# Kernel tuning notes

Hardware: AMD Instinct MI355X
Metric: run time of the kernel (lower is better)

The kernel has to match this reference:

```python
import jax, jax.numpy as jnp
import numpy as np

EPS = 1e-8
TEMP = 0.05

def setup_inputs() -> dict:
    key = jax.random.key(0)
    ks = jax.random.split(key, 7)
    B, S, IN, OUT, R, K = 4, 4096, 4096, 4096, 8, 4
    x = jax.random.normal(ks[0], (B, S, IN), dtype=jnp.float32)
    V_shared = jax.random.normal(ks[1], (R, IN), dtype=jnp.float32) * 0.01
    U_shared = jax.random.normal(ks[2], (OUT, R), dtype=jnp.float32) * 0.01
    core_pool = jax.random.normal(ks[3], (K, R, R), dtype=jnp.float32)
    core_keys = jax.random.normal(ks[4], (K, IN), dtype=jnp.float32)
    gate_w = jax.random.normal(ks[5], (1, 2 * R), dtype=jnp.float32) * 0.1
    gate_b = jnp.ones((1,), dtype=jnp.float32)
    return {"x": x, "V_shared": V_shared, "U_shared": U_shared,
            "core_pool": core_pool, "core_keys": core_keys,
            "gate_w": gate_w, "gate_b": gate_b}

def reference(x, V_shared, U_shared, core_pool, core_keys, gate_w, gate_b):
    # --- Hebbian cosine router (eval mode: keys are fixed buffers) ---
    centroid = 0.7 * x[:, -1, :] + 0.3 * jnp.mean(x, axis=1)          # [B, in]
    cn = centroid / jnp.maximum(jnp.linalg.norm(centroid, axis=-1, keepdims=True), EPS)
    kn = core_keys / jnp.maximum(jnp.linalg.norm(core_keys, axis=-1, keepdims=True), EPS)
    sim = cn @ kn.T                                                     # [B, K]
    route_weights = jax.nn.softmax(sim / TEMP, axis=-1)                 # [B, K]
    # --- Soft core mixture: per-batch rank x rank matrix ---
    Lam_active = jnp.einsum('bk,kij->bij', route_weights, core_pool)    # [B, r, r]
    # --- Low-rank chain: x @ V^T @ Lam^T @ U^T ---
    x_V = jnp.einsum('bsi,ri->bsr', x, V_shared)                        # [B, S, r]
    x_V_Lam = jnp.einsum('bsr,bjr->bsj', x_V, Lam_active)               # bmm with Lam^T
    adapt_out = jnp.einsum('bsj,oj->bso', x_V_Lam, U_shared)            # [B, S, out]
    # --- GainLoRA sigmoid gate (scalar), gate input detached ---
    gate_in = jax.lax.stop_gradient(
        jnp.concatenate([U_shared.mean(axis=0), V_shared.mean(axis=1)], axis=0))  # [2r]
    gate = jax.nn.sigmoid(gate_w @ gate_in + gate_b)                    # [1]
    return gate[0] * adapt_out
```

## Files before the change

### kernel.cpp

```cpp
#include <hip/hip_runtime.h>
#include <math.h>

#define B_   4
#define S_   4096
#define IN_  4096
#define OUT_ 4096
#define RNK  8
#define K_   4

#define NBLK_A 512

__global__ __launch_bounds__(256) void zK(float* __restrict__ p) {
    p[blockIdx.x * 256 + threadIdx.x] = 0.f;
}

__global__ __launch_bounds__(512) void kA(const float* __restrict__ x,
                                          const float* __restrict__ V,
                                          float* __restrict__ colsum,
                                          float* __restrict__ xv)
{
    __shared__ float shcs[IN_];
    const int tid = threadIdx.x;
    for (int c = tid; c < IN_; c += 512) shcs[c] = 0.f;
    __syncthreads();

    const int blk  = blockIdx.x;
    const int b    = blk >> 7;
    const int sblk = blk & 127;
    const int w = tid >> 6, l = tid & 63, g = l >> 4, j = l & 15;
    const int s = sblk * 32 + w * 4 + g;
    const float* xr = x + ((size_t)(b * S_ + s)) * IN_;

    float p[8] = {0.f,0.f,0.f,0.f,0.f,0.f,0.f,0.f};
    #pragma unroll 4
    for (int chunk = 0; chunk < 64; ++chunk) {
        const int col = chunk * 64 + j * 4;
        const float4 x4 = *(const float4*)(xr + col);
        #pragma unroll
        for (int r = 0; r < 8; ++r) {
            const float4 v4 = *(const float4*)(V + r * IN_ + col);
            p[r] += x4.x * v4.x + x4.y * v4.y + x4.z * v4.z + x4.w * v4.w;
        }
        float c0 = x4.x, c1 = x4.y, c2 = x4.z, c3 = x4.w;
        c0 += __shfl_xor(c0, 16); c1 += __shfl_xor(c1, 16);
        c2 += __shfl_xor(c2, 16); c3 += __shfl_xor(c3, 16);
        c0 += __shfl_xor(c0, 32); c1 += __shfl_xor(c1, 32);
        c2 += __shfl_xor(c2, 32); c3 += __shfl_xor(c3, 32);
        if (l < 16) {
            atomicAdd(&shcs[col + 0], c0);
            atomicAdd(&shcs[col + 1], c1);
            atomicAdd(&shcs[col + 2], c2);
            atomicAdd(&shcs[col + 3], c3);
        }
    }

    #pragma unroll
    for (int m = 1; m <= 8; m <<= 1) {
        #pragma unroll
        for (int r = 0; r < 8; ++r) p[r] += __shfl_xor(p[r], m);
    }
    float* xvp = xv + ((size_t)(b * S_ + s)) * RNK;
    if (j == 0) *(float4*)xvp       = make_float4(p[0], p[1], p[2], p[3]);
    if (j == 1) *(float4*)(xvp + 4) = make_float4(p[4], p[5], p[6], p[7]);

    __syncthreads();
    for (int c = tid; c < IN_; c += 512)
        unsafeAtomicAdd(&colsum[(size_t)b * IN_ + c], shcs[c]);
}

__global__ __launch_bounds__(256) void kB(const float* __restrict__ x,
                                          const float* __restrict__ V,
                                          const float* __restrict__ U,
                                          const float* __restrict__ core_pool,
                                          const float* __restrict__ core_keys,
                                          const float* __restrict__ gate_w,
                                          const float* __restrict__ gate_b,
                                          const float* __restrict__ colsum,
                                          float* __restrict__ P)
{
    const int b = blockIdx.x, tid = threadIdx.x;
    float nrm2 = 0.f;
    float dotk[K_] = {0.f,0.f,0.f,0.f};
    float kn2[K_]  = {0.f,0.f,0.f,0.f};
    float us[8] = {0.f,0.f,0.f,0.f,0.f,0.f,0.f,0.f};
    float vs[8] = {0.f,0.f,0.f,0.f,0.f,0.f,0.f,0.f};

    const float ms = 0.3f / (float)S_;
    for (int it = 0; it < 4; ++it) {
        const int c = it * 1024 + tid * 4;
        const float4 cs = *(const float4*)(colsum + (size_t)b * IN_ + c);
        const float4 xl = *(const float4*)(x + ((size_t)(b * S_ + S_ - 1)) * IN_ + c);
        float4 cen;
        cen.x = 0.7f * xl.x + ms * cs.x;
        cen.y = 0.7f * xl.y + ms * cs.y;
        cen.z = 0.7f * xl.z + ms * cs.z;
        cen.w = 0.7f * xl.w + ms * cs.w;
        nrm2 += cen.x*cen.x + cen.y*cen.y + cen.z*cen.z + cen.w*cen.w;
        #pragma unroll
        for (int k = 0; k < K_; ++k) {
            const float4 ck = *(const float4*)(core_keys + (size_t)k * IN_ + c);
            dotk[k] += cen.x*ck.x + cen.y*ck.y + cen.z*ck.z + cen.w*ck.w;
            kn2[k]  += ck.x*ck.x + ck.y*ck.y + ck.z*ck.z + ck.w*ck.w;
        }
    }
    for (int o = tid; o < OUT_; o += 256) {
        const float4 a  = *(const float4*)(U + (size_t)o * RNK);
        const float4 b4 = *(const float4*)(U + (size_t)o * RNK + 4);
        us[0]+=a.x;  us[1]+=a.y;  us[2]+=a.z;  us[3]+=a.w;
        us[4]+=b4.x; us[5]+=b4.y; us[6]+=b4.z; us[7]+=b4.w;
    }
    for (int it = 0; it < 4; ++it) {
        const int c = it * 1024 + tid * 4;
        #pragma unroll
        for (int r = 0; r < 8; ++r) {
            const float4 v = *(const float4*)(V + (size_t)r * IN_ + c);
            vs[r] += v.x + v.y + v.z + v.w;
        }
    }

    __shared__ float red[25 * 4];
    __shared__ float res[25];
    float vals[25];
    vals[0] = nrm2;
    #pragma unroll
    for (int k = 0; k < K_; ++k) { vals[1 + k] = dotk[k]; vals[5 + k] = kn2[k]; }
    #pragma unroll
    for (int r = 0; r < 8; ++r) { vals[9 + r] = us[r]; vals[17 + r] = vs[r]; }
    const int wid = tid >> 6, lane = tid & 63;
    #pragma unroll
    for (int i = 0; i < 25; ++i) {
        float v = vals[i];
        #pragma unroll
        for (int m = 32; m >= 1; m >>= 1) v += __shfl_xor(v, m);
        if (lane == 0) red[i * 4 + wid] = v;
    }
    __syncthreads();
    if (tid < 25) res[tid] = red[tid*4] + red[tid*4+1] + red[tid*4+2] + red[tid*4+3];
    __syncthreads();

    const float ncen = fmaxf(sqrtf(res[0]), 1e-8f);
    float lg[K_], mx = -1e30f;
    #pragma unroll
    for (int k = 0; k < K_; ++k) {
        const float nk = fmaxf(sqrtf(res[5 + k]), 1e-8f);
        lg[k] = (res[1 + k] / (ncen * nk)) * 20.0f;
        mx = fmaxf(mx, lg[k]);
    }
    float wk[K_], se = 0.f;
    #pragma unroll
    for (int k = 0; k < K_; ++k) { wk[k] = expf(lg[k] - mx); se += wk[k]; }
    const float inv_se = 1.f / se;
    float z = gate_b[0];
    #pragma unroll
    for (int r = 0; r < 8; ++r) z += gate_w[r]     * (res[9 + r]  * (1.f / OUT_));
    #pragma unroll
    for (int r = 0; r < 8; ++r) z += gate_w[8 + r] * (res[17 + r] * (1.f / IN_));
    const float gate = 1.f / (1.f + expf(-z));

    __shared__ float Tsh[64];
    if (tid < 64) {
        float acc = 0.f;
        #pragma unroll
        for (int k = 0; k < K_; ++k) acc += (wk[k] * inv_se) * core_pool[k * 64 + tid];
        Tsh[tid] = gate * acc;
    }
    __syncthreads();

    for (int o = tid; o < OUT_; o += 256) {
        const float4 a  = *(const float4*)(U + (size_t)o * RNK);
        const float4 b4 = *(const float4*)(U + (size_t)o * RNK + 4);
        const float u[8] = {a.x, a.y, a.z, a.w, b4.x, b4.y, b4.z, b4.w};
        float pr[8];
        #pragma unroll
        for (int r = 0; r < 8; ++r) {
            float acc = 0.f;
            #pragma unroll
            for (int jj = 0; jj < 8; ++jj) acc += u[jj] * Tsh[jj * 8 + r];
            pr[r] = acc;
        }
        *(float4*)(P + (size_t)(b * OUT_ + o) * RNK)     = make_float4(pr[0], pr[1], pr[2], pr[3]);
        *(float4*)(P + (size_t)(b * OUT_ + o) * RNK + 4) = make_float4(pr[4], pr[5], pr[6], pr[7]);
    }
}

__global__ __launch_bounds__(256) void kD(const float* __restrict__ P,
                                          const float* __restrict__ xv,
                                          float* __restrict__ out)
{
    const int blk = blockIdx.x;
    const int b = blk >> 9, rem = blk & 511;
    const int half = rem >> 8, sc = rem & 255;
    const int t = threadIdx.x;
    const int oA = half * 2048 + t * 4;

    float PA[4][8], PB[4][8];
    #pragma unroll
    for (int u = 0; u < 4; ++u) {
        const float* pp = P + ((size_t)(b * OUT_ + oA + u)) * RNK;
        const float4 a = *(const float4*)pp;
        const float4 c = *(const float4*)(pp + 4);
        PA[u][0]=a.x; PA[u][1]=a.y; PA[u][2]=a.z; PA[u][3]=a.w;
        PA[u][4]=c.x; PA[u][5]=c.y; PA[u][6]=c.z; PA[u][7]=c.w;
        const float* pq = pp + (size_t)1024 * RNK;
        const float4 d = *(const float4*)pq;
        const float4 e = *(const float4*)(pq + 4);
        PB[u][0]=d.x; PB[u][1]=d.y; PB[u][2]=d.z; PB[u][3]=d.w;
        PB[u][4]=e.x; PB[u][5]=e.y; PB[u][6]=e.z; PB[u][7]=e.w;
    }

    const int srow0 = sc * 16;
    const float* xvp = xv + ((size_t)(b * S_ + srow0)) * RNK;
    float* op = out + ((size_t)(b * S_ + srow0)) * OUT_ + oA;
    #pragma unroll 4
    for (int row = 0; row < 16; ++row) {
        const float4 xa = *(const float4*)(xvp + row * RNK);
        const float4 xb = *(const float4*)(xvp + row * RNK + 4);
        const float xr[8] = {xa.x, xa.y, xa.z, xa.w, xb.x, xb.y, xb.z, xb.w};
        float accA[4], accB[4];
        #pragma unroll
        for (int u = 0; u < 4; ++u) {
            float sA = 0.f, sB = 0.f;
            #pragma unroll
            for (int r = 0; r < 8; ++r) { sA += PA[u][r] * xr[r]; sB += PB[u][r] * xr[r]; }
            accA[u] = sA; accB[u] = sB;
        }
        *(float4*)(op + (size_t)row * OUT_)        = make_float4(accA[0], accA[1], accA[2], accA[3]);
        *(float4*)(op + (size_t)row * OUT_ + 1024) = make_float4(accB[0], accB[1], accB[2], accB[3]);
    }
}

extern "C" void kernel_launch(void* const* d_in, const int* in_sizes, int n_in,
                              void* d_out, int out_size, void* d_ws, size_t ws_size,
                              hipStream_t stream) {
    const float* x         = (const float*)d_in[0];
    const float* V         = (const float*)d_in[1];
    const float* U         = (const float*)d_in[2];
    const float* core_pool = (const float*)d_in[3];
    const float* core_keys = (const float*)d_in[4];
    const float* gate_w    = (const float*)d_in[5];
    const float* gate_b    = (const float*)d_in[6];
    float* out = (float*)d_out;

    float* colsum = (float*)d_ws;
    float* xv = colsum + (size_t)B_ * IN_;
    float* P  = xv + (size_t)B_ * S_ * RNK;

    zK<<<dim3((B_ * IN_) / 256), dim3(256), 0, stream>>>(colsum);
    kA<<<dim3(NBLK_A), dim3(512), 0, stream>>>(x, V, colsum, xv);
    kB<<<dim3(B_), dim3(256), 0, stream>>>(x, V, U, core_pool, core_keys,
                                           gate_w, gate_b, colsum, P);
    kD<<<dim3(2048), dim3(256), 0, stream>>>(P, xv, out);
}
```

Before: 602.7 us.

## Split input columns in half, stage V in LDS, process four rows per wave

The x-projection kernel now splits each row's input dimension into two halves across blocks, doubling the grid. Each block stages its slice of V in shared memory, and each wave processes four rows at once so V reads are reused and column sums need far fewer shared atomics. The two partial xV results go to separate buffers that the output kernel adds together. It also widens the routing kernel to 1024 threads and switches output stores to nontemporal. The cost is a larger workspace, 64KB of LDS per block that may limit occupancy, and extra xv reads in the output kernel.

```diff
diff --git a/kernel.cpp b/kernel.cpp
--- a/kernel.cpp
+++ b/kernel.cpp
@@ -8,75 +8,116 @@
 #define RNK  8
 #define K_   4
 
-#define NBLK_A 512
+#define HALFC 2048
+#define NKCH  8
+
+typedef float f4v __attribute__((ext_vector_type(4)));
 
 __global__ __launch_bounds__(256) void zK(float* __restrict__ p) {
     p[blockIdx.x * 256 + threadIdx.x] = 0.f;
 }
 
-__global__ __launch_bounds__(512) void kA(const float* __restrict__ x,
-                                          const float* __restrict__ V,
-                                          float* __restrict__ colsum,
-                                          float* __restrict__ xv)
+__global__ __launch_bounds__(512, 4) void kA(const float* __restrict__ x,
+                                             const float* __restrict__ V,
+                                             float* __restrict__ colsum,
+                                             float* __restrict__ xvp)
 {
-    __shared__ float shcs[IN_];
+    __shared__ float Vsh[RNK][HALFC];
+    __shared__ float shcs[4][512];
     const int tid = threadIdx.x;
-    for (int c = tid; c < IN_; c += 512) shcs[c] = 0.f;
-    __syncthreads();
 
     const int blk  = blockIdx.x;
-    const int b    = blk >> 7;
-    const int sblk = blk & 127;
-    const int w = tid >> 6, l = tid & 63, g = l >> 4, j = l & 15;
-    const int s = sblk * 32 + w * 4 + g;
-    const float* xr = x + ((size_t)(b * S_ + s)) * IN_;
-
-    float p[8] = {0.f,0.f,0.f,0.f,0.f,0.f,0.f,0.f};
-    #pragma unroll 4
-    for (int chunk = 0; chunk < 64; ++chunk) {
-        const int col = chunk * 64 + j * 4;
-        const float4 x4 = *(const float4*)(xr + col);
-        #pragma unroll
-        for (int r = 0; r < 8; ++r) {
-            const float4 v4 = *(const float4*)(V + r * IN_ + col);
-            p[r] += x4.x * v4.x + x4.y * v4.y + x4.z * v4.z + x4.w * v4.w;
-        }
-        float c0 = x4.x, c1 = x4.y, c2 = x4.z, c3 = x4.w;
-        c0 += __shfl_xor(c0, 16); c1 += __shfl_xor(c1, 16);
-        c2 += __shfl_xor(c2, 16); c3 += __shfl_xor(c3, 16);
-        c0 += __shfl_xor(c0, 32); c1 += __shfl_xor(c1, 32);
-        c2 += __shfl_xor(c2, 32); c3 += __shfl_xor(c3, 32);
-        if (l < 16) {
-            atomicAdd(&shcs[col + 0], c0);
-            atomicAdd(&shcs[col + 1], c1);
-            atomicAdd(&shcs[col + 2], c2);
-            atomicAdd(&shcs[col + 3], c3);
-        }
-    }
-
-    #pragma unroll
-    for (int m = 1; m <= 8; m <<= 1) {
-        #pragma unroll
-        for (int r = 0; r < 8; ++r) p[r] += __shfl_xor(p[r], m);
-    }
-    float* xvp = xv + ((size_t)(b * S_ + s)) * RNK;
-    if (j == 0) *(float4*)xvp       = make_float4(p[0], p[1], p[2], p[3]);
-    if (j == 1) *(float4*)(xvp + 4) = make_float4(p[4], p[5], p[6], p[7]);
-
-    __syncthreads();
-    for (int c = tid; c < IN_; c += 512)
-        unsafeAtomicAdd(&colsum[(size_t)b * IN_ + c], shcs[c]);
-}
-
-__global__ __launch_bounds__(256) void kB(const float* __restrict__ x,
-                                          const float* __restrict__ V,
-                                          const float* __restrict__ U,
-                                          const float* __restrict__ core_pool,
-                                          const float* __restrict__ core_keys,
-                                          const float* __restrict__ gate_w,
-                                          const float* __restrict__ gate_b,
-                                          const float* __restrict__ colsum,
-                                          float* __restrict__ P)
+    const int b    = blk >> 8;
+    const int rem  = blk & 255;
+    const int sblk = rem >> 1;
+    const int half = rem & 1;
+    const int c0   = half * HALFC;
+
+    for (int i = tid; i < 2048; i += 512) ((float*)shcs)[i] = 0.f;
+
+    for (int i = tid; i < (RNK * HALFC / 4); i += 512) {
+        const int r  = i >> 9;
+        const int cc = (i & 511) * 4;
+        *(float4*)&Vsh[r][cc] = *(const float4*)(V + (size_t)r * IN_ + c0 + cc);
+    }
+    __syncthreads();
+
+    const int w = tid >> 6, l = tid & 63;
+    const int s0 = sblk * 32 + w * 4;
+    const float* xb = x + ((size_t)(b * S_ + s0)) * IN_ + c0 + l * 4;
+
+    float acc[4][8];
+    #pragma unroll
+    for (int row = 0; row < 4; ++row)
+        #pragma unroll
+        for (int r = 0; r < 8; ++r) acc[row][r] = 0.f;
+
+    #pragma unroll 2
+    for (int k = 0; k < NKCH; ++k) {
+        const int col = k * 256 + l * 4;
+        float4 xr[4];
+        #pragma unroll
+        for (int row = 0; row < 4; ++row)
+            xr[row] = *(const float4*)(xb + (size_t)row * IN_ + k * 256);
+        float4 vr[8];
+        #pragma unroll
+        for (int r = 0; r < 8; ++r) vr[r] = *(const float4*)&Vsh[r][col];
+
+        #pragma unroll
+        for (int row = 0; row < 4; ++row) {
+            #pragma unroll
+            for (int r = 0; r < 8; ++r)
+                acc[row][r] += xr[row].x * vr[r].x + xr[row].y * vr[r].y
+                             + xr[row].z * vr[r].z + xr[row].w * vr[r].w;
+        }
+
+        const float c0s = xr[0].x + xr[1].x + xr[2].x + xr[3].x;
+        const float c1s = xr[0].y + xr[1].y + xr[2].y + xr[3].y;
+        const float c2s = xr[0].z + xr[1].z + xr[2].z + xr[3].z;
+        const float c3s = xr[0].w + xr[1].w + xr[2].w + xr[3].w;
+        const int q = k * 64 + l;
+        atomicAdd(&shcs[0][q], c0s);
+        atomicAdd(&shcs[1][q], c1s);
+        atomicAdd(&shcs[2][q], c2s);
+        atomicAdd(&shcs[3][q], c3s);
+    }
+
+    #pragma unroll
+    for (int m = 1; m <= 32; m <<= 1)
+        #pragma unroll
+        for (int row = 0; row < 4; ++row)
+            #pragma unroll
+            for (int r = 0; r < 8; ++r)
+                acc[row][r] += __shfl_xor(acc[row][r], m);
+
+    if (l == 0) {
+        float* xo = xvp + (size_t)half * (B_ * S_ * RNK)
+                        + ((size_t)(b * S_ + s0)) * RNK;
+        #pragma unroll
+        for (int row = 0; row < 4; ++row) {
+            *(float4*)(xo + row * RNK)     = make_float4(acc[row][0], acc[row][1],
+                                                         acc[row][2], acc[row][3]);
+            *(float4*)(xo + row * RNK + 4) = make_float4(acc[row][4], acc[row][5],
+                                                         acc[row][6], acc[row][7]);
+        }
+    }
+
+    __syncthreads();
+    for (int i = tid; i < 2048; i += 512) {
+        const int comp = i >> 9, q = i & 511;
+        unsafeAtomicAdd(&colsum[(size_t)b * IN_ + c0 + q * 4 + comp], ((float*)shcs)[i]);
+    }
+}
+
+__global__ __launch_bounds__(1024) void kB(const float* __restrict__ x,
+                                           const float* __restrict__ V,
+                                           const float* __restrict__ U,
+                                           const float* __restrict__ core_pool,
+                                           const float* __restrict__ core_keys,
+                                           const float* __restrict__ gate_w,
+                                           const float* __restrict__ gate_b,
+                                           const float* __restrict__ colsum,
+                                           float* __restrict__ P)
 {
     const int b = blockIdx.x, tid = threadIdx.x;
     float nrm2 = 0.f;
@@ -86,8 +127,8 @@
     float vs[8] = {0.f,0.f,0.f,0.f,0.f,0.f,0.f,0.f};
 
     const float ms = 0.3f / (float)S_;
-    for (int it = 0; it < 4; ++it) {
-        const int c = it * 1024 + tid * 4;
+    {
+        const int c = tid * 4;
         const float4 cs = *(const float4*)(colsum + (size_t)b * IN_ + c);
         const float4 xl = *(const float4*)(x + ((size_t)(b * S_ + S_ - 1)) * IN_ + c);
         float4 cen;
@@ -103,14 +144,14 @@
             kn2[k]  += ck.x*ck.x + ck.y*ck.y + ck.z*ck.z + ck.w*ck.w;
         }
     }
-    for (int o = tid; o < OUT_; o += 256) {
+    for (int o = tid; o < OUT_; o += 1024) {
         const float4 a  = *(const float4*)(U + (size_t)o * RNK);
         const float4 b4 = *(const float4*)(U + (size_t)o * RNK + 4);
         us[0]+=a.x;  us[1]+=a.y;  us[2]+=a.z;  us[3]+=a.w;
         us[4]+=b4.x; us[5]+=b4.y; us[6]+=b4.z; us[7]+=b4.w;
     }
-    for (int it = 0; it < 4; ++it) {
-        const int c = it * 1024 + tid * 4;
+    {
+        const int c = tid * 4;
         #pragma unroll
         for (int r = 0; r < 8; ++r) {
             const float4 v = *(const float4*)(V + (size_t)r * IN_ + c);
@@ -118,7 +159,7 @@
         }
     }
 
-    __shared__ float red[25 * 4];
+    __shared__ float red[25 * 16];
     __shared__ float res[25];
     float vals[25];
     vals[0] = nrm2;
@@ -132,10 +173,15 @@
         float v = vals[i];
         #pragma unroll
         for (int m = 32; m >= 1; m >>= 1) v += __shfl_xor(v, m);
-        if (lane == 0) red[i * 4 + wid] = v;
-    }
-    __syncthreads();
-    if (tid < 25) res[tid] = red[tid*4] + red[tid*4+1] + red[tid*4+2] + red[tid*4+3];
+        if (lane == 0) red[i * 16 + wid] = v;
+    }
+    __syncthreads();
+    if (tid < 25) {
+        float t = 0.f;
+        #pragma unroll
+        for (int j = 0; j < 16; ++j) t += red[tid * 16 + j];
+        res[tid] = t;
+    }
     __syncthreads();
 
     const float ncen = fmaxf(sqrtf(res[0]), 1e-8f);
@@ -166,7 +212,7 @@
     }
     __syncthreads();
 
-    for (int o = tid; o < OUT_; o += 256) {
+    for (int o = tid; o < OUT_; o += 1024) {
         const float4 a  = *(const float4*)(U + (size_t)o * RNK);
         const float4 b4 = *(const float4*)(U + (size_t)o * RNK + 4);
         const float u[8] = {a.x, a.y, a.z, a.w, b4.x, b4.y, b4.z, b4.w};
@@ -209,13 +255,17 @@
     }
 
     const int srow0 = sc * 16;
-    const float* xvp = xv + ((size_t)(b * S_ + srow0)) * RNK;
+    const float* xq0 = xv + ((size_t)(b * S_ + srow0)) * RNK;
+    const float* xq1 = xq0 + (size_t)(B_ * S_ * RNK);
     float* op = out + ((size_t)(b * S_ + srow0)) * OUT_ + oA;
     #pragma unroll 4
     for (int row = 0; row < 16; ++row) {
-        const float4 xa = *(const float4*)(xvp + row * RNK);
-        const float4 xb = *(const float4*)(xvp + row * RNK + 4);
-        const float xr[8] = {xa.x, xa.y, xa.z, xa.w, xb.x, xb.y, xb.z, xb.w};
+        const float4 xa = *(const float4*)(xq0 + row * RNK);
+        const float4 xb = *(const float4*)(xq0 + row * RNK + 4);
+        const float4 ya = *(const float4*)(xq1 + row * RNK);
+        const float4 yb = *(const float4*)(xq1 + row * RNK + 4);
+        const float xr[8] = {xa.x+ya.x, xa.y+ya.y, xa.z+ya.z, xa.w+ya.w,
+                             xb.x+yb.x, xb.y+yb.y, xb.z+yb.z, xb.w+yb.w};
         float accA[4], accB[4];
         #pragma unroll
         for (int u = 0; u < 4; ++u) {
@@ -224,8 +274,10 @@
             for (int r = 0; r < 8; ++r) { sA += PA[u][r] * xr[r]; sB += PB[u][r] * xr[r]; }
             accA[u] = sA; accB[u] = sB;
         }
-        *(float4*)(op + (size_t)row * OUT_)        = make_float4(accA[0], accA[1], accA[2], accA[3]);
-        *(float4*)(op + (size_t)row * OUT_ + 1024) = make_float4(accB[0], accB[1], accB[2], accB[3]);
+        f4v vA = {accA[0], accA[1], accA[2], accA[3]};
+        f4v vB = {accB[0], accB[1], accB[2], accB[3]};
+        __builtin_nontemporal_store(vA, (f4v*)(op + (size_t)row * OUT_));
+        __builtin_nontemporal_store(vB, (f4v*)(op + (size_t)row * OUT_ + 1024));
     }
 }
 
@@ -243,11 +295,11 @@
 
     float* colsum = (float*)d_ws;
     float* xv = colsum + (size_t)B_ * IN_;
-    float* P  = xv + (size_t)B_ * S_ * RNK;
+    float* P  = xv + (size_t)2 * B_ * S_ * RNK;
 
     zK<<<dim3((B_ * IN_) / 256), dim3(256), 0, stream>>>(colsum);
-    kA<<<dim3(NBLK_A), dim3(512), 0, stream>>>(x, V, colsum, xv);
-    kB<<<dim3(B_), dim3(256), 0, stream>>>(x, V, U, core_pool, core_keys,
-                                           gate_w, gate_b, colsum, P);
+    kA<<<dim3(1024), dim3(512), 0, stream>>>(x, V, colsum, xv);
+    kB<<<dim3(B_), dim3(1024), 0, stream>>>(x, V, U, core_pool, core_keys,
+                                            gate_w, gate_b, colsum, P);
     kD<<<dim3(2048), dim3(256), 0, stream>>>(P, xv, out);
 }
```

After: 495.9 us. 1.22x faster.
